# Kernel optimization log

Hardware: AMD Instinct MI355X
Metric: run time of the kernel (lower is better)

## Reference

```python
import jax, jax.numpy as jnp
import numpy as np

B, N_NUC, N_UP, N_DOWN = 512, 16, 32, 32
N_ELEC = N_UP + N_DOWN            # 64 electrons
F = 8                             # edge feature dim (Gaussian RBF envelopes)
D = N_NUC * F                     # embedding_dim = 128 (positional electron embeddings)
L = 3                             # n_interactions
N_ATOM_TYPES = 4


def _rbf(diff):
    # diff: [..., 3] -> [..., F]; Gaussian RBF features of the interparticle distance
    d = jnp.sqrt(jnp.sum(diff * diff, axis=-1) + 1e-12)
    mu = jnp.linspace(0.0, 4.0, F, dtype=diff.dtype)
    return jnp.exp(-(d[..., None] - mu) ** 2)


def setup_inputs() -> dict:
    key = jax.random.key(0)
    ks = jax.random.split(key, 9)
    r = 2.0 * jax.random.normal(ks[0], (B, N_ELEC, 3), dtype=jnp.float32)
    R = 2.0 * jax.random.normal(ks[1], (B, N_NUC, 3), dtype=jnp.float32)
    atom_types = jax.random.randint(ks[2], (N_NUC,), 0, N_ATOM_TYPES)
    embed_table = 0.1 * jax.random.normal(ks[3], (N_ATOM_TYPES, D), dtype=jnp.float32)
    we_same = 0.1 * jax.random.normal(ks[4], (L, F, D), dtype=jnp.float32)
    we_anti = 0.1 * jax.random.normal(ks[5], (L, F, D), dtype=jnp.float32)
    we_ne = 0.1 * jax.random.normal(ks[6], (L, F, D), dtype=jnp.float32)
    w_up = 0.05 * jax.random.normal(ks[7], (L, 4 * D, D), dtype=jnp.float32)
    b_up = jnp.zeros((L, D), dtype=jnp.float32)
    return {
        'r': r, 'R': R, 'embed_table': embed_table,
        'we_same': we_same, 'we_anti': we_anti, 'we_ne': we_ne,
        'w_up': w_up, 'b_up': b_up, 'atom_types': atom_types,
    }


def reference(r, R, embed_table, we_same, we_anti, we_ne, w_up, b_up, atom_types):
    # --- molecular graph edge construction (pairwise differences + edge features) ---
    ee_feat = _rbf(r[:, :, None, :] - r[:, None, :, :])   # [B, e, e, F]
    ne_feat = _rbf(r[:, :, None, :] - R[:, None, :, :])   # [B, e, n, F]

    spin = jnp.arange(N_ELEC) >= N_UP
    eye = jnp.eye(N_ELEC, dtype=bool)
    same_m = ((spin[:, None] == spin[None, :]) & ~eye).astype(ee_feat.dtype)  # no self-interaction
    anti_m = (spin[:, None] != spin[None, :]).astype(ee_feat.dtype)
    feat_same = ee_feat * same_m[None, :, :, None]
    feat_anti = ee_feat * anti_m[None, :, :, None]

    # --- node factory: positional electron embeddings (dense scatter of ne features == reshape) ---
    x = ne_feat.reshape(ne_feat.shape[0], N_ELEC, N_NUC * F)  # [B, e, D]
    y = embed_table[atom_types]                               # [n, D] nuclei embeddings

    # --- message-passing layers ---
    for l in range(L):
        # messages = Linear(edge_feats) * sender embedding, summed over senders per receiver;
        # contract sender axis first to keep intermediates at [B, e, F, D]
        t_s = jnp.einsum('bijf,bjd->bifd', feat_same, x)
        z_s = jnp.einsum('bifd,fd->bid', t_s, we_same[l])
        t_a = jnp.einsum('bijf,bjd->bifd', feat_anti, x)
        z_a = jnp.einsum('bifd,fd->bid', t_a, we_anti[l])
        t_n = jnp.einsum('binf,nd->bifd', ne_feat, y)
        z_n = jnp.einsum('bifd,fd->bid', t_n, we_ne[l])
        upd = jnp.concatenate([x, z_s, z_a, z_n], axis=-1)    # [B, e, 4D]
        x = x + jnp.tanh(upd @ w_up[l] + b_up[l])
    return x  # final electron embeddings [B, N_ELEC, D]
```

## Files before the change

### kernel.cpp

```cpp
#include <hip/hip_runtime.h>


typedef unsigned short u16;
typedef unsigned int u32;
typedef __attribute__((ext_vector_type(8))) short short8;
typedef __attribute__((ext_vector_type(4))) float f32x4;
typedef __attribute__((ext_vector_type(4))) u32 u32x4;
typedef _Float16 h2 __attribute__((ext_vector_type(2)));

__device__ __forceinline__ u16 f2h(float f){ return __builtin_bit_cast(u16, (_Float16)f); }
__device__ __forceinline__ float h2f(u16 a){ return (float)__builtin_bit_cast(_Float16, a); }

__device__ __forceinline__ short8 rbf8(float dd){
  short8 a;
#pragma unroll
  for (int f = 0; f < 8; f++){
    float u = dd - (4.0f/7.0f)*(float)f;
    a[f] = (short)f2h(__expf(-u*u));
  }
  return a;
}

__global__ __launch_bounds__(256) void gnn_prep(
    const float* __restrict__ w_up, const float* __restrict__ we_ne,
    const float* __restrict__ embed, const int* __restrict__ atypes,
    u16* __restrict__ wsegs){
  __shared__ u16 lw[16384];
  const int blk = blockIdx.x;
  const int l = blk / 5, seg = blk % 5;
  const int tid = threadIdx.x;
  if (seg < 4){
    const float* src = w_up + (l*512 + seg*128)*128;
#pragma unroll
    for (int mm = 0; mm < 16; mm++){
      int idx = mm*1024 + tid*4;
      float4 v = *(const float4*)(src + idx);
      lw[idx+0] = f2h(v.x); lw[idx+1] = f2h(v.y);
      lw[idx+2] = f2h(v.z); lw[idx+3] = f2h(v.w);
    }
  } else {
#pragma unroll
    for (int mm = 0; mm < 16; mm++){
      int idx = mm*1024 + tid*4;
      int k = idx >> 7, dout = idx & 127;
      int n = k >> 3, f = k & 7;
      float4 ye = *(const float4*)(embed + atypes[n]*128 + dout);
      float4 wn = *(const float4*)(we_ne + (l*8 + f)*128 + dout);
      lw[idx+0] = f2h(ye.x*wn.x); lw[idx+1] = f2h(ye.y*wn.y);
      lw[idx+2] = f2h(ye.z*wn.z); lw[idx+3] = f2h(ye.w*wn.w);
    }
  }
  __syncthreads();
  u16* dst = wsegs + blk*16384;
  const int col = tid & 15, q = (tid >> 4) & 3;
#pragma unroll
  for (int m = 0; m < 8; m++){
    int slot = m*4 + (tid >> 6);
    int c = slot >> 3, nt = slot & 7;
    int kbase = c*32 + q*8;
    int dout = nt*16 + col;
    short8 vv;
#pragma unroll
    for (int jj = 0; jj < 8; jj++) vv[jj] = (short)lw[(kbase+jj)*128 + dout];
    *(short8*)(dst + m*2048 + tid*8) = vv;
  }
}

__global__ __launch_bounds__(512, 2) void gnn_main(
    const float* __restrict__ r_g, const float* __restrict__ R_g,
    const float* __restrict__ weS_g, const float* __restrict__ weA_g,
    const float* __restrict__ bup_g,
    const u16* __restrict__ wsegs,
    float* __restrict__ out)
{
  extern __shared__ __attribute__((aligned(16))) u16 lds[];
  u16* const wb0 = lds;
  u16* const wb1 = lds + 16384;
  u16* const xbB = lds + 32768;
  u16* const zsB = lds + 50176;

  const int tid  = threadIdx.x;
  const int lane = tid & 63;
  const int w    = tid >> 6;
  const int bb   = w >> 2;
  const int wq   = w & 3;
  const int b    = blockIdx.x*2 + bb;
  const int col  = lane & 15;
  const int q    = lane >> 4;
  const int i0   = wq * 16;
  const int sp   = wq >> 1;
  const int mrow = i0 + col;
  const int loff = (q*16 + col) * 8;

  u16* const xb  = xbB + bb*8704;
  u16* const zst = zsB + bb*8704;

  u32x4 stg[4];
  auto stg_ld = [&](const u16* src){
#pragma unroll
    for (int m = 0; m < 4; m++) stg[m] = *(const u32x4*)(src + m*4096 + tid*8);
  };
  auto stg_st = [&](u16* dst){
#pragma unroll
    for (int m = 0; m < 4; m++) *(u32x4*)(dst + m*4096 + tid*8) = stg[m];
  };
  auto gemm_seg = [&](const u16* wbuf, const u16* arows, f32x4* acc){
#pragma unroll
    for (int c = 0; c < 4; c++){
      short8 a = *(const short8*)(arows + mrow*136 + c*32 + (q<<3));
#pragma unroll
      for (int nt = 0; nt < 8; nt++){
        short8 bf = *(const short8*)(wbuf + c*4096 + nt*512 + loff);
        acc[nt] = __builtin_amdgcn_mfma_f32_16x16x32_f16(a, bf, acc[nt], 0, 0, 0);
      }
    }
  };

  short8 aS[8], aA[8];
  float dN[4];
  {
    float* rs = (float*)(zsB + bb*8704);
    float* Rs = rs + 256;
    const int ht = tid & 255;
    if (ht < 64){
#pragma unroll
      for (int k = 0; k < 3; k++) rs[ht*4+k] = r_g[(b*64+ht)*3 + k];
    } else if (ht < 80){
      int n = ht - 64;
#pragma unroll
      for (int k = 0; k < 3; k++) Rs[n*4+k] = R_g[(b*16+n)*3 + k];
    }
    __syncthreads();
    {
      float x0 = rs[mrow*4], x1 = rs[mrow*4+1], x2 = rs[mrow*4+2];
#pragma unroll
      for (int c = 0; c < 8; c++){
        int j = 32*sp + 4*c + q;
        float dx = x0-rs[j*4], dy = x1-rs[j*4+1], dz = x2-rs[j*4+2];
        float dd = sqrtf(dx*dx + dy*dy + dz*dz + 1e-12f);
        aS[c] = rbf8(dd);
        if (j == mrow) aS[c] = (short8)0;
        j = 32*(1-sp) + 4*c + q;
        dx = x0-rs[j*4]; dy = x1-rs[j*4+1]; dz = x2-rs[j*4+2];
        aA[c] = rbf8(sqrtf(dx*dx + dy*dy + dz*dz + 1e-12f));
      }
#pragma unroll
      for (int c = 0; c < 4; c++){
        int n = 4*c + q;
        float dx = x0-Rs[n*4], dy = x1-Rs[n*4+1], dz = x2-Rs[n*4+2];
        dN[c] = sqrtf(dx*dx + dy*dy + dz*dz + 1e-12f);
      }
    }
    {
      int i = (tid & 255) >> 2, nb = (tid & 3)*4;
      float y0 = rs[i*4], y1 = rs[i*4+1], y2 = rs[i*4+2];
#pragma unroll
      for (int nn = 0; nn < 4; nn++){
        int n = nb + nn;
        float dx = y0-Rs[n*4], dy = y1-Rs[n*4+1], dz = y2-Rs[n*4+2];
        float dd = sqrtf(dx*dx + dy*dy + dz*dz + 1e-12f);
        *(short8*)&xb[i*136 + n*8] = rbf8(dd);
      }
    }
    stg_ld(wsegs + 0);
    stg_st(wb0);
    __syncthreads();
  }

  f32x4 xr[8];
#pragma unroll
  for (int nt = 0; nt < 8; nt++)
#pragma unroll
    for (int rr = 0; rr < 4; rr++)
      xr[nt][rr] = h2f(xb[(i0 + q*4 + rr)*136 + nt*16 + col]);

  const f32x4 vzero = {0.f, 0.f, 0.f, 0.f};

#pragma unroll 1
  for (int l = 0; l < 3; l++){
    const u16* slab = wsegs + l*81920;
    const int P = l & 1;
    u16* const bufA = P ? wb1 : wb0;
    u16* const bufB = P ? wb0 : wb1;

    float bupr[8];
#pragma unroll
    for (int nt = 0; nt < 8; nt++) bupr[nt] = bup_g[l*128 + nt*16 + col];

    f32x4 upd[8];
#pragma unroll
    for (int nt = 0; nt < 8; nt++) upd[nt] = vzero;

    auto zpass = [&](int pass){
      const float* weX = pass ? weA_g : weS_g;
      const int jb0 = pass ? 32*(1-sp) : 32*sp;
      const short8* aF = pass ? aA : aS;
      f32x4 zacc[8];
#pragma unroll
      for (int nt = 0; nt < 8; nt++) zacc[nt] = vzero;
#pragma unroll
      for (int nt = 0; nt < 8; nt++){
        h2 wp[4];
#pragma unroll
        for (int p = 0; p < 4; p++){
          h2 t;
          t[0] = (_Float16)weX[(l*8 + 2*p  )*128 + nt*16 + col];
          t[1] = (_Float16)weX[(l*8 + 2*p+1)*128 + nt*16 + col];
          wp[p] = t;
        }
        u16 xv[8];
#pragma unroll
        for (int c = 0; c < 8; c++) xv[c] = xb[(jb0 + 4*c + q)*136 + nt*16 + col];
#pragma unroll
        for (int c = 0; c < 8; c++){
          _Float16 xh = __builtin_bit_cast(_Float16, xv[c]);
          h2 xd; xd[0] = xh; xd[1] = xh;
          u32x4 bu;
#pragma unroll
          for (int p = 0; p < 4; p++)
            bu[p] = __builtin_bit_cast(u32, (h2)(xd * wp[p]));
          short8 bf = __builtin_bit_cast(short8, bu);
          zacc[nt] = __builtin_amdgcn_mfma_f32_16x16x32_f16(aF[c], bf, zacc[nt], 0, 0, 0);
        }
      }
#pragma unroll
      for (int nt = 0; nt < 8; nt++)
#pragma unroll
        for (int rr = 0; rr < 4; rr++)
          zst[(i0 + q*4 + rr)*136 + nt*16 + col] = f2h(zacc[nt][rr]);
    };

    stg_ld(slab + 1*16384);
    zpass(0);
    gemm_seg(bufA, xb, upd);
    stg_st(bufB); __syncthreads();
    stg_ld(slab + 2*16384);
    gemm_seg(bufB, zst, upd);
    stg_st(bufA); __syncthreads();
    stg_ld(slab + 4*16384);
    zpass(1);
    gemm_seg(bufA, zst, upd);
    stg_st(bufB); __syncthreads();
    stg_ld(slab + 3*16384);
    {
      f32x4 zn[8];
#pragma unroll
      for (int nt = 0; nt < 8; nt++) zn[nt] = vzero;
#pragma unroll
      for (int c = 0; c < 4; c++){
        short8 a = rbf8(dN[c]);
#pragma unroll
        for (int nt = 0; nt < 8; nt++){
          short8 bf = *(const short8*)(bufB + c*4096 + nt*512 + loff);
          zn[nt] = __builtin_amdgcn_mfma_f32_16x16x32_f16(a, bf, zn[nt], 0, 0, 0);
        }
      }
#pragma unroll
      for (int nt = 0; nt < 8; nt++)
#pragma unroll
        for (int rr = 0; rr < 4; rr++)
          zst[(i0 + q*4 + rr)*136 + nt*16 + col] = f2h(zn[nt][rr]);
    }
    stg_st(bufA); __syncthreads();
    if (l < 2) stg_ld(slab + 81920);
    gemm_seg(bufA, zst, upd);
#pragma unroll
    for (int nt = 0; nt < 8; nt++){
#pragma unroll
      for (int rr = 0; rr < 4; rr++){
        float v = upd[nt][rr] + bupr[nt];
        float e = __expf(2.0f * v);
        float th = 1.0f - 2.0f * __builtin_amdgcn_rcpf(e + 1.0f);
        xr[nt][rr] += th;
      }
    }
    if (l < 2){
#pragma unroll
      for (int nt = 0; nt < 8; nt++)
#pragma unroll
        for (int rr = 0; rr < 4; rr++)
          xb[(i0 + q*4 + rr)*136 + nt*16 + col] = f2h(xr[nt][rr]);
      stg_st(bufB);
      __syncthreads();
    } else {
#pragma unroll
      for (int nt = 0; nt < 8; nt++)
#pragma unroll
        for (int rr = 0; rr < 4; rr++)
          out[(b*64 + i0 + q*4 + rr)*128 + nt*16 + col] = xr[nt][rr];
    }
  }
}

extern "C" void kernel_launch(void* const* d_in, const int* in_sizes, int n_in,
                              void* d_out, int out_size, void* d_ws, size_t ws_size,
                              hipStream_t stream){
  const float* r     = (const float*)d_in[0];
  const float* R     = (const float*)d_in[1];
  const float* embed = (const float*)d_in[2];
  const float* weS   = (const float*)d_in[3];
  const float* weA   = (const float*)d_in[4];
  const float* weN   = (const float*)d_in[5];
  const float* wup   = (const float*)d_in[6];
  const float* bup   = (const float*)d_in[7];
  const int* atyp    = (const int*)d_in[8];

  u16* wsegs = (u16*)d_ws;

  (void)hipFuncSetAttribute((const void*)gnn_main,
                            hipFuncAttributeMaxDynamicSharedMemorySize, 135168);
  gnn_prep<<<15, 256, 0, stream>>>(wup, weN, embed, atyp, wsegs);
  gnn_main<<<256, 512, 135168, stream>>>(r, R, weS, weA, bup, wsegs, (float*)d_out);
}
```

Baseline: 136.4 us.

## Split output columns across wave halves, one batch per block, single weight buffer

Each block now handles one batch element instead of two. The 8 waves split the 128 output columns into two halves of 4 tiles each, instead of splitting by batch. The double-buffered weight staging is replaced with a single LDS buffer guarded by extra barriers, which cuts LDS to about 66KB and allows 4 blocks per CU with 512 blocks launched. This trades more barriers and less load/compute overlap for higher occupancy and fewer registers per wave. The z-pass elementwise weight scaling and the A-fragment RBF setup are now duplicated across both column halves.

```diff
diff --git a/kernel.cpp b/kernel.cpp
--- a/kernel.cpp
+++ b/kernel.cpp
@@ -66,7 +66,7 @@
   }
 }
 
-__global__ __launch_bounds__(512, 2) void gnn_main(
+__global__ __launch_bounds__(512, 4) void gnn_main(
     const float* __restrict__ r_g, const float* __restrict__ R_g,
     const float* __restrict__ weS_g, const float* __restrict__ weA_g,
     const float* __restrict__ bup_g,
@@ -74,44 +74,41 @@
     float* __restrict__ out)
 {
   extern __shared__ __attribute__((aligned(16))) u16 lds[];
-  u16* const wb0 = lds;
-  u16* const wb1 = lds + 16384;
-  u16* const xbB = lds + 32768;
-  u16* const zsB = lds + 50176;
+  u16* const wbuf = lds;
+  u16* const xb   = lds + 16384;
+  u16* const zst  = lds + 16384 + 8704;
 
   const int tid  = threadIdx.x;
+  const int b    = blockIdx.x;
   const int lane = tid & 63;
   const int w    = tid >> 6;
-  const int bb   = w >> 2;
   const int wq   = w & 3;
-  const int b    = blockIdx.x*2 + bb;
+  const int nh   = w >> 2;
   const int col  = lane & 15;
   const int q    = lane >> 4;
   const int i0   = wq * 16;
   const int sp   = wq >> 1;
   const int mrow = i0 + col;
   const int loff = (q*16 + col) * 8;
-
-  u16* const xb  = xbB + bb*8704;
-  u16* const zst = zsB + bb*8704;
+  const int ntb  = nh * 4;
 
   u32x4 stg[4];
   auto stg_ld = [&](const u16* src){
 #pragma unroll
     for (int m = 0; m < 4; m++) stg[m] = *(const u32x4*)(src + m*4096 + tid*8);
   };
-  auto stg_st = [&](u16* dst){
-#pragma unroll
-    for (int m = 0; m < 4; m++) *(u32x4*)(dst + m*4096 + tid*8) = stg[m];
+  auto stg_st = [&](){
+#pragma unroll
+    for (int m = 0; m < 4; m++) *(u32x4*)(wbuf + m*4096 + tid*8) = stg[m];
   };
-  auto gemm_seg = [&](const u16* wbuf, const u16* arows, f32x4* acc){
+  auto gemm4 = [&](const u16* arows, f32x4* acc){
 #pragma unroll
     for (int c = 0; c < 4; c++){
       short8 a = *(const short8*)(arows + mrow*136 + c*32 + (q<<3));
 #pragma unroll
-      for (int nt = 0; nt < 8; nt++){
-        short8 bf = *(const short8*)(wbuf + c*4096 + nt*512 + loff);
-        acc[nt] = __builtin_amdgcn_mfma_f32_16x16x32_f16(a, bf, acc[nt], 0, 0, 0);
+      for (int ntl = 0; ntl < 4; ntl++){
+        short8 bf = *(const short8*)(wbuf + c*4096 + (ntb+ntl)*512 + loff);
+        acc[ntl] = __builtin_amdgcn_mfma_f32_16x16x32_f16(a, bf, acc[ntl], 0, 0, 0);
       }
     }
   };
@@ -119,14 +116,13 @@
   short8 aS[8], aA[8];
   float dN[4];
   {
-    float* rs = (float*)(zsB + bb*8704);
+    float* rs = (float*)zst;
     float* Rs = rs + 256;
-    const int ht = tid & 255;
-    if (ht < 64){
-#pragma unroll
-      for (int k = 0; k < 3; k++) rs[ht*4+k] = r_g[(b*64+ht)*3 + k];
-    } else if (ht < 80){
-      int n = ht - 64;
+    if (tid < 64){
+#pragma unroll
+      for (int k = 0; k < 3; k++) rs[tid*4+k] = r_g[(b*64+tid)*3 + k];
+    } else if (tid < 80){
+      int n = tid - 64;
 #pragma unroll
       for (int k = 0; k < 3; k++) Rs[n*4+k] = R_g[(b*16+n)*3 + k];
     }
@@ -152,10 +148,10 @@
       }
     }
     {
-      int i = (tid & 255) >> 2, nb = (tid & 3)*4;
+      int i = tid >> 3, nb = (tid & 7)*2;
       float y0 = rs[i*4], y1 = rs[i*4+1], y2 = rs[i*4+2];
 #pragma unroll
-      for (int nn = 0; nn < 4; nn++){
+      for (int nn = 0; nn < 2; nn++){
         int n = nb + nn;
         float dx = y0-Rs[n*4], dy = y1-Rs[n*4+1], dz = y2-Rs[n*4+2];
         float dd = sqrtf(dx*dx + dy*dy + dz*dz + 1e-12f);
@@ -163,43 +159,41 @@
       }
     }
     stg_ld(wsegs + 0);
-    stg_st(wb0);
+    stg_st();
     __syncthreads();
-  }
-
-  f32x4 xr[8];
-#pragma unroll
-  for (int nt = 0; nt < 8; nt++)
+    stg_ld(wsegs + 16384);
+  }
+
+  f32x4 xr[4];
+#pragma unroll
+  for (int ntl = 0; ntl < 4; ntl++)
 #pragma unroll
     for (int rr = 0; rr < 4; rr++)
-      xr[nt][rr] = h2f(xb[(i0 + q*4 + rr)*136 + nt*16 + col]);
+      xr[ntl][rr] = h2f(xb[(i0 + q*4 + rr)*136 + (ntb+ntl)*16 + col]);
 
   const f32x4 vzero = {0.f, 0.f, 0.f, 0.f};
 
 #pragma unroll 1
   for (int l = 0; l < 3; l++){
     const u16* slab = wsegs + l*81920;
-    const int P = l & 1;
-    u16* const bufA = P ? wb1 : wb0;
-    u16* const bufB = P ? wb0 : wb1;
-
-    float bupr[8];
-#pragma unroll
-    for (int nt = 0; nt < 8; nt++) bupr[nt] = bup_g[l*128 + nt*16 + col];
-
-    f32x4 upd[8];
-#pragma unroll
-    for (int nt = 0; nt < 8; nt++) upd[nt] = vzero;
+    float bupr[4];
+#pragma unroll
+    for (int ntl = 0; ntl < 4; ntl++) bupr[ntl] = bup_g[l*128 + (ntb+ntl)*16 + col];
+
+    f32x4 upd[4];
+#pragma unroll
+    for (int ntl = 0; ntl < 4; ntl++) upd[ntl] = vzero;
 
     auto zpass = [&](int pass){
       const float* weX = pass ? weA_g : weS_g;
       const int jb0 = pass ? 32*(1-sp) : 32*sp;
       const short8* aF = pass ? aA : aS;
-      f32x4 zacc[8];
-#pragma unroll
-      for (int nt = 0; nt < 8; nt++) zacc[nt] = vzero;
-#pragma unroll
-      for (int nt = 0; nt < 8; nt++){
+      f32x4 zacc[4];
+#pragma unroll
+      for (int ntl = 0; ntl < 4; ntl++) zacc[ntl] = vzero;
+#pragma unroll
+      for (int ntl = 0; ntl < 4; ntl++){
+        int nt = ntb + ntl;
         h2 wp[4];
 #pragma unroll
         for (int p = 0; p < 4; p++){
@@ -220,74 +214,69 @@
           for (int p = 0; p < 4; p++)
             bu[p] = __builtin_bit_cast(u32, (h2)(xd * wp[p]));
           short8 bf = __builtin_bit_cast(short8, bu);
-          zacc[nt] = __builtin_amdgcn_mfma_f32_16x16x32_f16(aF[c], bf, zacc[nt], 0, 0, 0);
+          zacc[ntl] = __builtin_amdgcn_mfma_f32_16x16x32_f16(aF[c], bf, zacc[ntl], 0, 0, 0);
         }
       }
 #pragma unroll
-      for (int nt = 0; nt < 8; nt++)
+      for (int ntl = 0; ntl < 4; ntl++)
 #pragma unroll
         for (int rr = 0; rr < 4; rr++)
-          zst[(i0 + q*4 + rr)*136 + nt*16 + col] = f2h(zacc[nt][rr]);
+          zst[(i0 + q*4 + rr)*136 + (ntb+ntl)*16 + col] = f2h(zacc[ntl][rr]);
     };
 
-    stg_ld(slab + 1*16384);
     zpass(0);
-    gemm_seg(bufA, xb, upd);
-    stg_st(bufB); __syncthreads();
-    stg_ld(slab + 2*16384);
-    gemm_seg(bufB, zst, upd);
-    stg_st(bufA); __syncthreads();
-    stg_ld(slab + 4*16384);
+    gemm4(xb, upd);
+    __syncthreads(); stg_st(); stg_ld(slab + 4*16384); __syncthreads();
+    gemm4(zst, upd);
+    __syncthreads(); stg_st(); stg_ld(slab + 2*16384); __syncthreads();
     zpass(1);
-    gemm_seg(bufA, zst, upd);
-    stg_st(bufB); __syncthreads();
-    stg_ld(slab + 3*16384);
-    {
-      f32x4 zn[8];
-#pragma unroll
-      for (int nt = 0; nt < 8; nt++) zn[nt] = vzero;
-#pragma unroll
-      for (int c = 0; c < 4; c++){
-        short8 a = rbf8(dN[c]);
-#pragma unroll
-        for (int nt = 0; nt < 8; nt++){
-          short8 bf = *(const short8*)(bufB + c*4096 + nt*512 + loff);
-          zn[nt] = __builtin_amdgcn_mfma_f32_16x16x32_f16(a, bf, zn[nt], 0, 0, 0);
-        }
-      }
-#pragma unroll
-      for (int nt = 0; nt < 8; nt++)
-#pragma unroll
-        for (int rr = 0; rr < 4; rr++)
-          zst[(i0 + q*4 + rr)*136 + nt*16 + col] = f2h(zn[nt][rr]);
-    }
-    stg_st(bufA); __syncthreads();
+    f32x4 zn[4];
+#pragma unroll
+    for (int ntl = 0; ntl < 4; ntl++) zn[ntl] = vzero;
+#pragma unroll
+    for (int c = 0; c < 4; c++){
+      short8 a = rbf8(dN[c]);
+#pragma unroll
+      for (int ntl = 0; ntl < 4; ntl++){
+        short8 bf = *(const short8*)(wbuf + c*4096 + (ntb+ntl)*512 + loff);
+        zn[ntl] = __builtin_amdgcn_mfma_f32_16x16x32_f16(a, bf, zn[ntl], 0, 0, 0);
+      }
+    }
+    __syncthreads(); stg_st(); stg_ld(slab + 3*16384); __syncthreads();
+    gemm4(zst, upd);
+    __syncthreads(); stg_st();
     if (l < 2) stg_ld(slab + 81920);
-    gemm_seg(bufA, zst, upd);
-#pragma unroll
-    for (int nt = 0; nt < 8; nt++){
+    __syncthreads();
+#pragma unroll
+    for (int ntl = 0; ntl < 4; ntl++)
+#pragma unroll
+      for (int rr = 0; rr < 4; rr++)
+        zst[(i0 + q*4 + rr)*136 + (ntb+ntl)*16 + col] = f2h(zn[ntl][rr]);
+    __syncthreads();
+    gemm4(zst, upd);
+#pragma unroll
+    for (int ntl = 0; ntl < 4; ntl++){
 #pragma unroll
       for (int rr = 0; rr < 4; rr++){
-        float v = upd[nt][rr] + bupr[nt];
+        float v = upd[ntl][rr] + bupr[ntl];
         float e = __expf(2.0f * v);
         float th = 1.0f - 2.0f * __builtin_amdgcn_rcpf(e + 1.0f);
-        xr[nt][rr] += th;
+        xr[ntl][rr] += th;
       }
     }
     if (l < 2){
 #pragma unroll
-      for (int nt = 0; nt < 8; nt++)
+      for (int ntl = 0; ntl < 4; ntl++)
 #pragma unroll
         for (int rr = 0; rr < 4; rr++)
-          xb[(i0 + q*4 + rr)*136 + nt*16 + col] = f2h(xr[nt][rr]);
-      stg_st(bufB);
-      __syncthreads();
+          xb[(i0 + q*4 + rr)*136 + (ntb+ntl)*16 + col] = f2h(xr[ntl][rr]);
+      __syncthreads(); stg_st(); stg_ld(slab + 81920 + 16384); __syncthreads();
     } else {
 #pragma unroll
-      for (int nt = 0; nt < 8; nt++)
+      for (int ntl = 0; ntl < 4; ntl++)
 #pragma unroll
         for (int rr = 0; rr < 4; rr++)
-          out[(b*64 + i0 + q*4 + rr)*128 + nt*16 + col] = xr[nt][rr];
+          out[(b*64 + i0 + q*4 + rr)*128 + (ntb+ntl)*16 + col] = xr[ntl][rr];
     }
   }
 }
@@ -308,7 +297,7 @@
   u16* wsegs = (u16*)d_ws;
 
   (void)hipFuncSetAttribute((const void*)gnn_main,
-                            hipFuncAttributeMaxDynamicSharedMemorySize, 135168);
+                            hipFuncAttributeMaxDynamicSharedMemorySize, 67584);
   gnn_prep<<<15, 256, 0, stream>>>(wup, weN, embed, atyp, wsegs);
-  gnn_main<<<256, 512, 135168, stream>>>(r, R, weS, weA, bup, wsegs, (float*)d_out);
+  gnn_main<<<512, 512, 67584, stream>>>(r, R, weS, weA, bup, wsegs, (float*)d_out);
 }
```

Result: slower. 205.4 us (+50.7%).
